# Optimization experiments

Measured on AMD Instinct MI355X. Metric: run time of the kernel, lower is better.

## Reference

```python
import jax, jax.numpy as jnp
import numpy as np

N = 50000       # nodes
E = 800000      # edges (before self-loops)
IN_DIM = 128
HID = 64
HEADS = 4
C = HID // HEADS  # 16 per-head channels
NEG_SLOPE = 0.2   # PyG GATConv default
BN_EPS = 1e-5


def setup_inputs() -> dict:
    key = jax.random.key(0)
    ks = jax.random.split(key, 16)
    inp = {
        "x": jax.random.normal(ks[0], (N, IN_DIM), jnp.float32),
        "edge_index": jax.random.randint(ks[1], (2, E), 0, N, dtype=jnp.int32),
    }
    def glorot(k, shape):
        fan = sum(shape)
        return jax.random.normal(k, shape, jnp.float32) * jnp.sqrt(2.0 / fan)
    # layer 0: in=IN_DIM, layer 1: in=HID
    inp["W0"] = glorot(ks[2], (IN_DIM, HEADS * C))
    inp["a_src0"] = glorot(ks[3], (HEADS, C))
    inp["a_dst0"] = glorot(ks[4], (HEADS, C))
    inp["b0"] = jnp.zeros((HEADS * C,), jnp.float32)
    inp["g0"] = jnp.ones((HID,), jnp.float32)
    inp["be0"] = jnp.zeros((HID,), jnp.float32)
    inp["W1"] = glorot(ks[5], (HID, HEADS * C))
    inp["a_src1"] = glorot(ks[6], (HEADS, C))
    inp["a_dst1"] = glorot(ks[7], (HEADS, C))
    inp["b1"] = jnp.zeros((HEADS * C,), jnp.float32)
    inp["g1"] = jnp.ones((HID,), jnp.float32)
    inp["be1"] = jnp.zeros((HID,), jnp.float32)
    return inp


def _segment_softmax(e, dst, n):
    # softmax over edges grouped by destination node, per head. e: [Et, H]
    m = jax.ops.segment_max(e, dst, num_segments=n)          # [N, H]
    ex = jnp.exp(e - m[dst])
    s = jax.ops.segment_sum(ex, dst, num_segments=n)         # [N, H]
    return ex / (s[dst] + 1e-16)


def _gat_conv(h, src, dst, W, a_s, a_d, b):
    n = h.shape[0]
    hp = (h @ W).reshape(n, HEADS, C)                        # [N, H, C]
    al_s = jnp.einsum('nhc,hc->nh', hp, a_s)                 # [N, H]
    al_d = jnp.einsum('nhc,hc->nh', hp, a_d)
    e = jax.nn.leaky_relu(al_s[src] + al_d[dst], NEG_SLOPE)  # [Et, H]
    alpha = _segment_softmax(e, dst, n)
    msg = hp[src] * alpha[:, :, None]                        # [Et, H, C]
    out = jax.ops.segment_sum(msg, dst, num_segments=n)      # [N, H, C]
    return out.reshape(n, HEADS * C) + b


def _batch_norm(h, g, b):
    mu = h.mean(axis=0)
    var = h.var(axis=0)
    return (h - mu) * jax.lax.rsqrt(var + BN_EPS) * g + b


def reference(x, edge_index, W0, a_src0, a_dst0, b0, g0, be0,
              W1, a_src1, a_dst1, b1, g1, be1):
    n = x.shape[0]
    loops = jnp.arange(n, dtype=edge_index.dtype)
    src = jnp.concatenate([edge_index[0], loops])  # PyG adds self-loops
    dst = jnp.concatenate([edge_index[1], loops])
    h = _gat_conv(x, src, dst, W0, a_src0, a_dst0, b0)
    h = _batch_norm(h, g0, be0)
    h = jax.nn.relu(h)  # dropout: identity (eval / deterministic)
    h = _gat_conv(h, src, dst, W1, a_src1, a_dst1, b1)
    h = _batch_norm(h, g1, be1)
    return h
```

## Files before the change

kernel.cpp:

```cpp
#include <hip/hip_runtime.h>
#include <hip/hip_fp16.h>

#define CAP 128

__device__ __forceinline__ float sel4(float4 v, int h) {
  return h == 0 ? v.x : h == 1 ? v.y : h == 2 ? v.z : v.w;
}

template<int K, bool APPLY_BN>
__global__ void __launch_bounds__(256, 4)
gemm_tiled(const float* __restrict__ X, const float* __restrict__ W,
           const float* __restrict__ a_s, const float* __restrict__ a_d,
           const float* __restrict__ bnsum, const float* __restrict__ bnsq,
           const float* __restrict__ g, const float* __restrict__ be,
           __half* __restrict__ hp, float* __restrict__ al_s,
           float* __restrict__ al_d, int n)
{
  __shared__ float Wl[(K / 4) * 64 * 4];
  __shared__ float Xt[64 * K];

  for (int gi = threadIdx.x; gi < (K / 4) * 64; gi += 256) {
    int k4 = gi >> 6, ln = gi & 63;
    float4 w;
    w.x = W[(k4 * 4 + 0) * 64 + ln];
    w.y = W[(k4 * 4 + 1) * 64 + ln];
    w.z = W[(k4 * 4 + 2) * 64 + ln];
    w.w = W[(k4 * 4 + 3) * 64 + ln];
    *(float4*)&Wl[gi * 4] = w;
  }

  int row0 = blockIdx.x * 64;
  int nrows = min(64, n - row0);
  float4 sc, sh;
  if (APPLY_BN) {
    int cg = (threadIdx.x & 15) * 4;
    float inv_n = 1.f / (float)n;
#pragma unroll
    for (int q = 0; q < 4; ++q) {
      float mu  = bnsum[cg + q] * inv_n;
      float var = bnsq[cg + q] * inv_n - mu * mu;
      float s   = g[cg + q] * rsqrtf(var + 1e-5f);
      ((float*)&sc)[q] = s;
      ((float*)&sh)[q] = be[cg + q] - mu * s;
    }
  }
  const float4* src = (const float4*)(X + (size_t)row0 * K);
  int nf4 = nrows * (K / 4);
  for (int i = threadIdx.x; i < nf4; i += 256) {
    float4 v = src[i];
    if (APPLY_BN) {
      v.x = fmaxf(v.x * sc.x + sh.x, 0.f);
      v.y = fmaxf(v.y * sc.y + sh.y, 0.f);
      v.z = fmaxf(v.z * sc.z + sh.z, 0.f);
      v.w = fmaxf(v.w * sc.w + sh.w, 0.f);
    }
    *(float4*)&Xt[i * 4] = v;
  }
  __syncthreads();

  int lane = threadIdx.x & 63;
  int wid  = threadIdx.x >> 6;
  int rbase = wid * 16;
  float acc[16];
#pragma unroll
  for (int r = 0; r < 16; ++r) acc[r] = 0.f;

  for (int k4 = 0; k4 < K / 4; ++k4) {
    float4 wv = *(const float4*)&Wl[(k4 * 64 + lane) * 4];
#pragma unroll
    for (int r = 0; r < 16; ++r) {
      float4 xv = *(const float4*)&Xt[(rbase + r) * K + k4 * 4];
      acc[r] += xv.x * wv.x + xv.y * wv.y + xv.z * wv.z + xv.w * wv.w;
    }
  }

  float as_l = a_s[lane], ad_l = a_d[lane];
  int h = lane >> 4, c = lane & 15;
#pragma unroll
  for (int r = 0; r < 16; ++r) {
    int lr = rbase + r;
    if (lr >= nrows) break;
    int row = row0 + lr;
    float a = acc[r];
    hp[(size_t)row * 64 + lane] = __float2half(a);
    float vs = a * as_l;
    float vd = a * ad_l;
#pragma unroll
    for (int off = 8; off >= 1; off >>= 1) {
      vs += __shfl_xor(vs, off, 64);
      vd += __shfl_xor(vd, off, 64);
    }
    if (c == 0) { al_s[row * 4 + h] = vs; al_d[row * 4 + h] = vd; }
  }
}

__global__ void hist_k(const int* __restrict__ ei, int E, int N, int* __restrict__ count)
{
  int e = blockIdx.x * 256 + threadIdx.x;
  int Et = E + N;
  if (e >= Et) return;
  int d = (e < E) ? ei[E + e] : (e - E);
  atomicAdd(&count[d], 1);
}

__global__ void scan_block_k(const int* __restrict__ count, int* __restrict__ row_ptr,
                             int* __restrict__ partial, int n)
{
  __shared__ int woff[16];
  int tid = threadIdx.x;
  int i = blockIdx.x * 1024 + tid;
  int v = (i < n) ? count[i] : 0;
  int lane = tid & 63, wid = tid >> 6;
  int incl = v;
#pragma unroll
  for (int off = 1; off < 64; off <<= 1) {
    int t = __shfl_up(incl, off, 64);
    if (lane >= off) incl += t;
  }
  if (lane == 63) woff[wid] = incl;
  __syncthreads();
  if (tid < 16) {
    int wv = woff[tid];
    int winc = wv;
#pragma unroll
    for (int off = 1; off < 16; off <<= 1) {
      int t = __shfl_up(winc, off, 64);
      if (tid >= off) winc += t;
    }
    woff[tid] = winc - wv;
    if (tid == 15) partial[blockIdx.x] = winc;
  }
  __syncthreads();
  if (i < n) row_ptr[i] = woff[wid] + incl - v;
}

__global__ void scan_partial_k(int* __restrict__ partial, int* __restrict__ row_ptr,
                               int nb, int n)
{
  int tid = threadIdx.x;
  int v = (tid < nb) ? partial[tid] : 0;
  int incl = v;
#pragma unroll
  for (int off = 1; off < 64; off <<= 1) {
    int t = __shfl_up(incl, off, 64);
    if (tid >= off) incl += t;
  }
  if (tid < nb) partial[tid] = incl - v;
  if (tid == 63) row_ptr[n] = incl;
}

__global__ void scan_add_k(int* __restrict__ row_ptr, int* __restrict__ cursor,
                           const int* __restrict__ partial, int n)
{
  int i = blockIdx.x * 1024 + threadIdx.x;
  if (i < n) {
    int r = row_ptr[i] + partial[blockIdx.x];
    row_ptr[i] = r;
    cursor[i] = r;
  }
}

__global__ void scatter_k(const int* __restrict__ ei, int E, int N,
                          int* __restrict__ cursor, int* __restrict__ col_src)
{
  int e = blockIdx.x * 256 + threadIdx.x;
  int Et = E + N;
  if (e >= Et) return;
  int s, d;
  if (e < E) { s = ei[e]; d = ei[E + e]; } else { s = d = e - E; }
  int pos = atomicAdd(&cursor[d], 1);
  col_src[pos] = s;
}

__global__ void __launch_bounds__(256)
ew_den_k(const int* __restrict__ row_ptr, const int* __restrict__ col_src,
         const float* __restrict__ al_s, const float* __restrict__ al_d,
         float4* __restrict__ ew4, float4* __restrict__ den4, int n)
{
  int lane = threadIdx.x & 63;
  int wid  = threadIdx.x >> 6;
  int nwaves = gridDim.x * 4;
  for (int d = blockIdx.x * 4 + wid; d < n; d += nwaves) {
    int beg = row_ptr[d], end = row_ptr[d + 1];
    int deg = end - beg;
    float4 ald4 = *(const float4*)(al_d + (size_t)d * 4);
    float s0 = 0.f, s1 = 0.f, s2 = 0.f, s3 = 0.f;
    for (int jb = 0; jb < deg; jb += 64) {
      int jj = jb + lane;
      if (jj < deg) {
        int s = col_src[beg + jj];
        float4 a = *(const float4*)(al_s + (size_t)s * 4);
        float ex = a.x + ald4.x; ex = ex >= 0.f ? ex : 0.2f * ex;
        float ey = a.y + ald4.y; ey = ey >= 0.f ? ey : 0.2f * ey;
        float ez = a.z + ald4.z; ez = ez >= 0.f ? ez : 0.2f * ez;
        float ew = a.w + ald4.w; ew = ew >= 0.f ? ew : 0.2f * ew;
        ex = __expf(ex); ey = __expf(ey); ez = __expf(ez); ew = __expf(ew);
        ew4[beg + jj] = make_float4(ex, ey, ez, ew);
        s0 += ex; s1 += ey; s2 += ez; s3 += ew;
      }
    }
#pragma unroll
    for (int off = 32; off >= 1; off >>= 1) {
      s0 += __shfl_xor(s0, off, 64);
      s1 += __shfl_xor(s1, off, 64);
      s2 += __shfl_xor(s2, off, 64);
      s3 += __shfl_xor(s3, off, 64);
    }
    if (lane == 0) den4[d] = make_float4(s0, s1, s2, s3);
  }
}

__global__ void __launch_bounds__(256)
node_agg(const int* __restrict__ row_ptr, const int* __restrict__ col_src,
         const float4* __restrict__ ew4, const float4* __restrict__ den4,
         const __half* __restrict__ hp, const float* __restrict__ bias,
         float* __restrict__ hpre, float* __restrict__ bnsum, float* __restrict__ bnsq,
         int n)
{
  __shared__ int   sh_s[4][CAP];
  __shared__ float sh_w[4][CAP * 4];
  __shared__ float sh_o[4][64];
  __shared__ float shs[64], shq[64];

  int lane = threadIdx.x & 63;
  int wid  = threadIdx.x >> 6;
  int c    = lane & 31;
  int e2   = lane >> 5;
  int h    = c >> 3;
  float b  = bias[lane];
  float lsum = 0.f, lsq = 0.f;
  int nwaves = gridDim.x * 4;

  for (int d = blockIdx.x * 4 + wid; d < n; d += nwaves) {
    int beg = row_ptr[d], end = row_ptr[d + 1];
    int deg = end - beg;
    float4 dn = den4[d];
    float acc0 = 0.f, acc1 = 0.f;

    if (deg <= CAP) {
      int degR = (deg + 15) & ~15;
      for (int jb = 0; jb < degR; jb += 64) {
        int jj = jb + lane;
        if (jj < deg) {
          sh_s[wid][jj] = col_src[beg + jj];
          *(float4*)&sh_w[wid][jj * 4] = ew4[beg + jj];
        } else if (jj < degR) {
          sh_s[wid][jj] = 0;
          *(float4*)&sh_w[wid][jj * 4] = make_float4(0.f, 0.f, 0.f, 0.f);
        }
      }
      __builtin_amdgcn_wave_barrier();
      for (int j = 0; j < degR; j += 16) {
#pragma unroll
        for (int k = 0; k < 8; ++k) {
          int e = j + k * 2 + e2;
          int s = sh_s[wid][e];
          float wh = sh_w[wid][e * 4 + h];
          unsigned raw = *(const unsigned*)(hp + (size_t)s * 64 + c * 2);
          float2 f = __half22float2(*(const __half2*)&raw);
          acc0 += wh * f.x;
          acc1 += wh * f.y;
        }
      }
      acc0 += __shfl_xor(acc0, 32, 64);
      acc1 += __shfl_xor(acc1, 32, 64);
    } else {
      for (int j = beg; j < end; ++j) {
        int s = col_src[j];
        float wh = sel4(ew4[j], h);
        unsigned raw = *(const unsigned*)(hp + (size_t)s * 64 + c * 2);
        float2 f = __half22float2(*(const __half2*)&raw);
        acc0 += wh * f.x;
        acc1 += wh * f.y;
      }
    }

    if (lane < 32) *(float2*)&sh_o[wid][c * 2] = make_float2(acc0, acc1);
    __builtin_amdgcn_wave_barrier();
    float den = sel4(dn, lane >> 4);
    float outv = sh_o[wid][lane] / (den + 1e-16f) + b;

    hpre[(size_t)d * 64 + lane] = outv;
    lsum += outv; lsq += outv * outv;
  }

  if (threadIdx.x < 64) { shs[threadIdx.x] = 0.f; shq[threadIdx.x] = 0.f; }
  __syncthreads();
  atomicAdd(&shs[lane], lsum);
  atomicAdd(&shq[lane], lsq);
  __syncthreads();
  if (threadIdx.x < 64) {
    atomicAdd(&bnsum[threadIdx.x], shs[threadIdx.x]);
    atomicAdd(&bnsq[threadIdx.x],  shq[threadIdx.x]);
  }
}

__global__ void bn_apply(float* __restrict__ buf, const float* __restrict__ bnsum,
                         const float* __restrict__ bnsq, const float* __restrict__ g,
                         const float* __restrict__ be, int n)
{
  size_t i = (size_t)blockIdx.x * 256 + threadIdx.x;
  size_t total = (size_t)n * 64;
  if (i >= total) return;
  int c = (int)(i & 63);
  float inv_n = 1.f / (float)n;
  float mu  = bnsum[c] * inv_n;
  float var = bnsq[c] * inv_n - mu * mu;
  buf[i] = (buf[i] - mu) * rsqrtf(var + 1e-5f) * g[c] + be[c];
}

extern "C" void kernel_launch(void* const* d_in, const int* in_sizes, int n_in,
                              void* d_out, int out_size, void* d_ws, size_t ws_size,
                              hipStream_t stream) {
  const float* x   = (const float*)d_in[0];
  const int*   ei  = (const int*)d_in[1];
  const float* W0  = (const float*)d_in[2];
  const float* as0 = (const float*)d_in[3];
  const float* ad0 = (const float*)d_in[4];
  const float* b0  = (const float*)d_in[5];
  const float* g0  = (const float*)d_in[6];
  const float* be0 = (const float*)d_in[7];
  const float* W1  = (const float*)d_in[8];
  const float* as1 = (const float*)d_in[9];
  const float* ad1 = (const float*)d_in[10];
  const float* b1  = (const float*)d_in[11];
  const float* g1  = (const float*)d_in[12];
  const float* be1 = (const float*)d_in[13];
  float* out = (float*)d_out;

  int N = in_sizes[0] / 128;
  int E = in_sizes[1] / 2;
  int Et = E + N;

  char* w = (char*)d_ws;
  auto alloc = [&](size_t bytes) {
    char* p = w; w += (bytes + 255) & ~255ull; return p;
  };
  int*    count = (int*)alloc((size_t)N * 4 + 4 * 64 * 4);
  float*  bnsum0 = (float*)(count + N);
  float*  bnsq0  = bnsum0 + 64;
  float*  bnsum1 = bnsq0 + 64;
  float*  bnsq1  = bnsum1 + 64;
  __half* hp    = (__half*)alloc((size_t)N * 64 * 2);
  float*  hpre0 = (float*)alloc((size_t)N * 64 * 4);
  float*  als   = (float*)alloc((size_t)N * 4 * 4);
  float*  ald   = (float*)alloc((size_t)N * 4 * 4);
  int*    rowp  = (int*)alloc((size_t)(N + 1) * 4);
  int*    cursor= (int*)alloc((size_t)N * 4);
  int*    parts = (int*)alloc(64 * 4);
  int*    csrc  = (int*)alloc((size_t)Et * 4);
  float4* ew4   = (float4*)alloc((size_t)Et * 16);
  float4* den4  = (float4*)alloc((size_t)N * 16);

  dim3 blk(256);
  int gEt   = (Et + 255) / 256;
  int gN64  = (N * 64 + 255) / 256;
  int nb    = (N + 1023) / 1024;
  int gTile = (N + 63) / 64;

  hipMemsetAsync(count, 0, (size_t)N * 4 + 4 * 64 * 4, stream);

  hist_k<<<gEt, blk, 0, stream>>>(ei, E, N, count);
  scan_block_k<<<nb, 1024, 0, stream>>>(count, rowp, parts, N);
  scan_partial_k<<<1, 64, 0, stream>>>(parts, rowp, nb, N);
  scan_add_k<<<nb, 1024, 0, stream>>>(rowp, cursor, parts, N);
  scatter_k<<<gEt, blk, 0, stream>>>(ei, E, N, cursor, csrc);

  gemm_tiled<128, false><<<gTile, blk, 0, stream>>>(x, W0, as0, ad0,
                                                    nullptr, nullptr, nullptr, nullptr,
                                                    hp, als, ald, N);
  ew_den_k<<<2048, blk, 0, stream>>>(rowp, csrc, als, ald, ew4, den4, N);
  node_agg<<<2048, blk, 0, stream>>>(rowp, csrc, ew4, den4, hp, b0,
                                     hpre0, bnsum0, bnsq0, N);

  gemm_tiled<64, true><<<gTile, blk, 0, stream>>>(hpre0, W1, as1, ad1,
                                                  bnsum0, bnsq0, g0, be0,
                                                  hp, als, ald, N);
  ew_den_k<<<2048, blk, 0, stream>>>(rowp, csrc, als, ald, ew4, den4, N);
  node_agg<<<2048, blk, 0, stream>>>(rowp, csrc, ew4, den4, hp, b1,
                                     out, bnsum1, bnsq1, N);
  bn_apply<<<gN64, blk, 0, stream>>>(out, bnsum1, bnsq1, g1, be1, N);
}
```

Baseline: 349.1 us.

## Fuse attention-weight and softmax-denominator computation into the aggregation kernel

Removes the separate ew_den_k pass and computes the exp'd leaky-relu edge scores and per-head softmax denominators inside node_agg, while it gathers the source indices. This drops the Et×16-byte edge-weight buffer, the per-node denominator buffer and one launch per layer, cutting global write and read traffic. It also adds nontemporal hints on the col_src loads and the hpre stores. The trade-off is that the exp work now sits on the aggregation kernel's critical path, and nontemporal stores may hurt reuse of hpre0 by the next GEMM.

```diff
diff --git a/kernel.cpp b/kernel.cpp
--- a/kernel.cpp
+++ b/kernel.cpp
@@ -173,68 +173,31 @@
 }
 
 __global__ void __launch_bounds__(256)
-ew_den_k(const int* __restrict__ row_ptr, const int* __restrict__ col_src,
+node_agg(const int* __restrict__ row_ptr, const int* __restrict__ col_src,
          const float* __restrict__ al_s, const float* __restrict__ al_d,
-         float4* __restrict__ ew4, float4* __restrict__ den4, int n)
-{
+         const __half* __restrict__ hp, const float* __restrict__ bias,
+         float* __restrict__ hpre, float* __restrict__ bnsum, float* __restrict__ bnsq,
+         int n)
+{
+  __shared__ int   sh_s[4][CAP];
+  __shared__ float sh_w[4][CAP * 4];
+  __shared__ float sh_o[4][64];
+  __shared__ float shs[64], shq[64];
+
   int lane = threadIdx.x & 63;
   int wid  = threadIdx.x >> 6;
+  int c    = lane & 31;
+  int e2   = lane >> 5;
+  int h4   = c >> 3;
+  float b  = bias[lane];
+  float lsum = 0.f, lsq = 0.f;
   int nwaves = gridDim.x * 4;
+
   for (int d = blockIdx.x * 4 + wid; d < n; d += nwaves) {
     int beg = row_ptr[d], end = row_ptr[d + 1];
     int deg = end - beg;
     float4 ald4 = *(const float4*)(al_d + (size_t)d * 4);
-    float s0 = 0.f, s1 = 0.f, s2 = 0.f, s3 = 0.f;
-    for (int jb = 0; jb < deg; jb += 64) {
-      int jj = jb + lane;
-      if (jj < deg) {
-        int s = col_src[beg + jj];
-        float4 a = *(const float4*)(al_s + (size_t)s * 4);
-        float ex = a.x + ald4.x; ex = ex >= 0.f ? ex : 0.2f * ex;
-        float ey = a.y + ald4.y; ey = ey >= 0.f ? ey : 0.2f * ey;
-        float ez = a.z + ald4.z; ez = ez >= 0.f ? ez : 0.2f * ez;
-        float ew = a.w + ald4.w; ew = ew >= 0.f ? ew : 0.2f * ew;
-        ex = __expf(ex); ey = __expf(ey); ez = __expf(ez); ew = __expf(ew);
-        ew4[beg + jj] = make_float4(ex, ey, ez, ew);
-        s0 += ex; s1 += ey; s2 += ez; s3 += ew;
-      }
-    }
-#pragma unroll
-    for (int off = 32; off >= 1; off >>= 1) {
-      s0 += __shfl_xor(s0, off, 64);
-      s1 += __shfl_xor(s1, off, 64);
-      s2 += __shfl_xor(s2, off, 64);
-      s3 += __shfl_xor(s3, off, 64);
-    }
-    if (lane == 0) den4[d] = make_float4(s0, s1, s2, s3);
-  }
-}
-
-__global__ void __launch_bounds__(256)
-node_agg(const int* __restrict__ row_ptr, const int* __restrict__ col_src,
-         const float4* __restrict__ ew4, const float4* __restrict__ den4,
-         const __half* __restrict__ hp, const float* __restrict__ bias,
-         float* __restrict__ hpre, float* __restrict__ bnsum, float* __restrict__ bnsq,
-         int n)
-{
-  __shared__ int   sh_s[4][CAP];
-  __shared__ float sh_w[4][CAP * 4];
-  __shared__ float sh_o[4][64];
-  __shared__ float shs[64], shq[64];
-
-  int lane = threadIdx.x & 63;
-  int wid  = threadIdx.x >> 6;
-  int c    = lane & 31;
-  int e2   = lane >> 5;
-  int h    = c >> 3;
-  float b  = bias[lane];
-  float lsum = 0.f, lsq = 0.f;
-  int nwaves = gridDim.x * 4;
-
-  for (int d = blockIdx.x * 4 + wid; d < n; d += nwaves) {
-    int beg = row_ptr[d], end = row_ptr[d + 1];
-    int deg = end - beg;
-    float4 dn = den4[d];
+    float p0 = 0.f, p1 = 0.f, p2 = 0.f, p3 = 0.f;
     float acc0 = 0.f, acc1 = 0.f;
 
     if (deg <= CAP) {
@@ -242,20 +205,35 @@
       for (int jb = 0; jb < degR; jb += 64) {
         int jj = jb + lane;
         if (jj < deg) {
-          sh_s[wid][jj] = col_src[beg + jj];
-          *(float4*)&sh_w[wid][jj * 4] = ew4[beg + jj];
+          int s = __builtin_nontemporal_load(&col_src[beg + jj]);
+          float4 a = *(const float4*)(al_s + (size_t)s * 4);
+          float ex = a.x + ald4.x; ex = ex >= 0.f ? ex : 0.2f * ex;
+          float ey = a.y + ald4.y; ey = ey >= 0.f ? ey : 0.2f * ey;
+          float ez = a.z + ald4.z; ez = ez >= 0.f ? ez : 0.2f * ez;
+          float ew = a.w + ald4.w; ew = ew >= 0.f ? ew : 0.2f * ew;
+          ex = __expf(ex); ey = __expf(ey); ez = __expf(ez); ew = __expf(ew);
+          sh_s[wid][jj] = s;
+          *(float4*)&sh_w[wid][jj * 4] = make_float4(ex, ey, ez, ew);
+          p0 += ex; p1 += ey; p2 += ez; p3 += ew;
         } else if (jj < degR) {
           sh_s[wid][jj] = 0;
           *(float4*)&sh_w[wid][jj * 4] = make_float4(0.f, 0.f, 0.f, 0.f);
         }
       }
+#pragma unroll
+      for (int off = 32; off >= 1; off >>= 1) {
+        p0 += __shfl_xor(p0, off, 64);
+        p1 += __shfl_xor(p1, off, 64);
+        p2 += __shfl_xor(p2, off, 64);
+        p3 += __shfl_xor(p3, off, 64);
+      }
       __builtin_amdgcn_wave_barrier();
       for (int j = 0; j < degR; j += 16) {
 #pragma unroll
         for (int k = 0; k < 8; ++k) {
           int e = j + k * 2 + e2;
           int s = sh_s[wid][e];
-          float wh = sh_w[wid][e * 4 + h];
+          float wh = sh_w[wid][e * 4 + h4];
           unsigned raw = *(const unsigned*)(hp + (size_t)s * 64 + c * 2);
           float2 f = __half22float2(*(const __half2*)&raw);
           acc0 += wh * f.x;
@@ -267,7 +245,15 @@
     } else {
       for (int j = beg; j < end; ++j) {
         int s = col_src[j];
-        float wh = sel4(ew4[j], h);
+        float4 a = *(const float4*)(al_s + (size_t)s * 4);
+        float ex = a.x + ald4.x; ex = ex >= 0.f ? ex : 0.2f * ex;
+        float ey = a.y + ald4.y; ey = ey >= 0.f ? ey : 0.2f * ey;
+        float ez = a.z + ald4.z; ez = ez >= 0.f ? ez : 0.2f * ez;
+        float ew = a.w + ald4.w; ew = ew >= 0.f ? ew : 0.2f * ew;
+        ex = __expf(ex); ey = __expf(ey); ez = __expf(ez); ew = __expf(ew);
+        p0 += ex; p1 += ey; p2 += ez; p3 += ew;
+        float4 w4 = make_float4(ex, ey, ez, ew);
+        float wh = sel4(w4, h4);
         unsigned raw = *(const unsigned*)(hp + (size_t)s * 64 + c * 2);
         float2 f = __half22float2(*(const __half2*)&raw);
         acc0 += wh * f.x;
@@ -277,10 +263,10 @@
 
     if (lane < 32) *(float2*)&sh_o[wid][c * 2] = make_float2(acc0, acc1);
     __builtin_amdgcn_wave_barrier();
-    float den = sel4(dn, lane >> 4);
+    float den = (lane < 16) ? p0 : (lane < 32) ? p1 : (lane < 48) ? p2 : p3;
     float outv = sh_o[wid][lane] / (den + 1e-16f) + b;
 
-    hpre[(size_t)d * 64 + lane] = outv;
+    __builtin_nontemporal_store(outv, &hpre[(size_t)d * 64 + lane]);
     lsum += outv; lsq += outv * outv;
   }
 
@@ -349,8 +335,6 @@
   int*    cursor= (int*)alloc((size_t)N * 4);
   int*    parts = (int*)alloc(64 * 4);
   int*    csrc  = (int*)alloc((size_t)Et * 4);
-  float4* ew4   = (float4*)alloc((size_t)Et * 16);
-  float4* den4  = (float4*)alloc((size_t)N * 16);
 
   dim3 blk(256);
   int gEt   = (Et + 255) / 256;
@@ -369,15 +353,13 @@
   gemm_tiled<128, false><<<gTile, blk, 0, stream>>>(x, W0, as0, ad0,
                                                     nullptr, nullptr, nullptr, nullptr,
                                                     hp, als, ald, N);
-  ew_den_k<<<2048, blk, 0, stream>>>(rowp, csrc, als, ald, ew4, den4, N);
-  node_agg<<<2048, blk, 0, stream>>>(rowp, csrc, ew4, den4, hp, b0,
+  node_agg<<<2048, blk, 0, stream>>>(rowp, csrc, als, ald, hp, b0,
                                      hpre0, bnsum0, bnsq0, N);
 
   gemm_tiled<64, true><<<gTile, blk, 0, stream>>>(hpre0, W1, as1, ad1,
                                                   bnsum0, bnsq0, g0, be0,
                                                   hp, als, ald, N);
-  ew_den_k<<<2048, blk, 0, stream>>>(rowp, csrc, als, ald, ew4, den4, N);
-  node_agg<<<2048, blk, 0, stream>>>(rowp, csrc, ew4, den4, hp, b1,
+  node_agg<<<2048, blk, 0, stream>>>(rowp, csrc, als, ald, hp, b1,
                                      out, bnsum1, bnsq1, N);
   bn_apply<<<gN64, blk, 0, stream>>>(out, bnsum1, bnsq1, g1, be1, N);
 }
```

Result: faster. 325.8 us, median of 2 (-6.7%).
